# Kernel optimization log

Hardware: AMD Instinct MI355X
Metric: run time of the kernel (lower is better)

The kernel has to match this reference:

```python
import jax, jax.numpy as jnp
import numpy as np

B, S, H, I, A = 1024, 200, 256, 256, 128


def setup_inputs() -> dict:
    key = jax.random.key(0)
    ks = jax.random.split(key, 9)
    def xavier(k, shape):
        fan_in, fan_out = shape[1], shape[0]
        std = float(np.sqrt(2.0 / (fan_in + fan_out)))
        return jax.random.normal(k, shape, dtype=jnp.float32) * std
    return {
        "hidden_states": jax.random.normal(ks[0], (B, S, H), dtype=jnp.float32),
        "target_item": jax.random.normal(ks[1], (B, I), dtype=jnp.float32),
        "lengths": jax.random.randint(ks[2], (B,), 0, 201, dtype=jnp.int32),
        "W1": xavier(ks[3], (A, I + H)),
        "b1": jnp.zeros((A,), dtype=jnp.float32),
        "W2": xavier(ks[4], (1, A)),
        "Wr": xavier(ks[5], (H, I + H)),
        "br": jnp.zeros((H,), dtype=jnp.float32),
        "Wz": xavier(ks[6], (H, I + H)),
        "bz": jnp.zeros((H,), dtype=jnp.float32),
        "Wn": xavier(ks[7], (H, I + H)),
        "bn": jnp.zeros((H,), dtype=jnp.float32),
    }


def reference(hidden_states, target_item, lengths, W1, b1, W2, Wr, br, Wz, bz, Wn, bn):
    b, s, h = hidden_states.shape
    # attention scores over the sequence
    tgt = jnp.broadcast_to(target_item[:, None, :], (b, s, target_item.shape[-1]))
    combined = jnp.concatenate([hidden_states, tgt], axis=2)          # (B,S,2H)
    hid = jax.nn.relu(jnp.einsum('bsd,ad->bsa', combined, W1) + b1)   # (B,S,A)
    scores = jnp.einsum('bsa,oa->bs', hid, W2)                        # (B,S)
    mask = jnp.arange(s)[None, :] < lengths[:, None]
    scores = jnp.where(mask, scores, -1e9)
    att = jax.nn.softmax(scores, axis=1)                              # (B,S)

    def step(h_prev, xs):
        x, a = xs  # x: (B,I), a: (B,1)
        comb = jnp.concatenate([x, h_prev], axis=1)
        r = jax.nn.sigmoid(comb @ Wr.T + br)
        z = jax.nn.sigmoid(comb @ Wz.T + bz) * a
        comb_r = jnp.concatenate([x, r * h_prev], axis=1)
        n = jnp.tanh(comb_r @ Wn.T + bn)
        h_new = (1.0 - z) * h_prev + z * n
        return h_new, None

    h0 = jnp.zeros((b, h), dtype=hidden_states.dtype)
    xs = (jnp.transpose(hidden_states, (1, 0, 2)), att.T[:, :, None])  # (S,B,I),(S,B,1)
    h_final, _ = jax.lax.scan(step, h0, xs)
    return h_final
```

## Files before the change

kernel.cpp:

```cpp
#include <hip/hip_runtime.h>
#include <cstdint>

#define B_SZ  1024
#define S_LEN 200
#define H_DIM 256

typedef short s16x8 __attribute__((ext_vector_type(8)));
typedef float f32x4 __attribute__((ext_vector_type(4)));
typedef int   i32x4 __attribute__((ext_vector_type(4)));

__device__ __forceinline__ short f2bf(float f){
  uint32_t u = __float_as_uint(f);
  u += 0x7FFFu + ((u >> 16) & 1u);
  return (short)(u >> 16);
}
__device__ __forceinline__ float sigm(float x){
  return __fdividef(1.f, 1.f + __expf(-x));
}
__device__ __forceinline__ float tanh_f(float x){
  return 1.f - __fdividef(2.f, __expf(2.f*x) + 1.f);
}

__global__ __launch_bounds__(256) void prep_kernel(
    const float* __restrict__ Wr, const float* __restrict__ Wz,
    const float* __restrict__ Wn, const float* __restrict__ W1,
    short* __restrict__ wx, short* __restrict__ wrzh,
    short* __restrict__ wnh, short* __restrict__ w1b){
  const int NWX=196608, NRZ=131072, NN=65536;
  int i = blockIdx.x*256 + threadIdx.x;
  if(i < NWX){
    int o=i>>8, k=i&255;
    float v = (o<256)? Wr[o*512+k] : (o<512)? Wz[(o-256)*512+k] : Wn[(o-512)*512+k];
    wx[i]=f2bf(v);
  } else if(i < NWX+NRZ){
    int j=i-NWX; int o=j>>8, k=j&255;
    float v=(o<256)? Wr[o*512+256+k] : Wz[(o-256)*512+256+k];
    wrzh[j]=f2bf(v);
  } else if(i < NWX+NRZ+NN){
    int j=i-NWX-NRZ; int o=j>>8, k=j&255;
    wnh[j]=f2bf(Wn[o*512+256+k]);
  } else {
    int j=i-NWX-NRZ-NN;
    w1b[j]=f2bf(W1[j]);
  }
}

__global__ __launch_bounds__(256) void scores_kernel(
    const float* __restrict__ hs, const float* __restrict__ tgt,
    const short* __restrict__ w1, const float* __restrict__ b1,
    const float* __restrict__ w2, float* __restrict__ scores){
  const int tid = threadIdx.x;
  const int lane = tid & 63;
  const int wv  = tid >> 6;
  const int l15 = lane & 15;
  const int q   = lane >> 4;
  const int gw  = blockIdx.x * 4 + wv;
  float b1v[8], w2v[8];
  #pragma unroll
  for(int nt=0;nt<8;nt++){ b1v[nt]=b1[nt*16+l15]; w2v[nt]=w2[nt*16+l15]; }
  const short* w1p = w1 + (size_t)l15*512 + q*8;
  for(int it=0; it<2; it++){
    int mt0 = gw + it*3200;
    int mt1 = mt0 + 6400;
    int m0  = mt0*16 + l15;
    int m1  = mt1*16 + l15;
    int bA  = m0 / S_LEN, sA = m0 - bA*S_LEN;
    int bB  = m1 / S_LEN, sB = m1 - bB*S_LEN;
    const float* arowA = hs  + ((size_t)bA*S_LEN + sA)*H_DIM;
    const float* trowA = tgt + (size_t)bA*H_DIM;
    const float* arowB = hs  + ((size_t)bB*S_LEN + sB)*H_DIM;
    const float* trowB = tgt + (size_t)bB*H_DIM;
    f32x4 acc[2][8];
    #pragma unroll
    for(int u=0;u<2;u++)
      #pragma unroll
      for(int nt=0;nt<8;nt++) acc[u][nt] = (f32x4){0.f,0.f,0.f,0.f};
    for(int kt=0;kt<16;kt++){
      int k0 = kt*32 + q*8;
      const float* srcA = (k0 < H_DIM) ? (arowA + k0) : (trowA + (k0 - H_DIM));
      const float* srcB = (k0 < H_DIM) ? (arowB + k0) : (trowB + (k0 - H_DIM));
      float4 a0 = *(const float4*)(srcA);
      float4 a1 = *(const float4*)(srcA+4);
      float4 c0 = *(const float4*)(srcB);
      float4 c1 = *(const float4*)(srcB+4);
      s16x8 aA, aB;
      aA[0]=f2bf(a0.x); aA[1]=f2bf(a0.y); aA[2]=f2bf(a0.z); aA[3]=f2bf(a0.w);
      aA[4]=f2bf(a1.x); aA[5]=f2bf(a1.y); aA[6]=f2bf(a1.z); aA[7]=f2bf(a1.w);
      aB[0]=f2bf(c0.x); aB[1]=f2bf(c0.y); aB[2]=f2bf(c0.z); aB[3]=f2bf(c0.w);
      aB[4]=f2bf(c1.x); aB[5]=f2bf(c1.y); aB[6]=f2bf(c1.z); aB[7]=f2bf(c1.w);
      #pragma unroll
      for(int nt=0;nt<8;nt++){
        s16x8 bf = *(const s16x8*)(w1p + (size_t)nt*16*512 + kt*32);
        acc[0][nt] = __builtin_amdgcn_mfma_f32_16x16x32_bf16(aA, bf, acc[0][nt], 0, 0, 0);
        acc[1][nt] = __builtin_amdgcn_mfma_f32_16x16x32_bf16(aB, bf, acc[1][nt], 0, 0, 0);
      }
    }
    #pragma unroll
    for(int u=0;u<2;u++){
      float sr0=0.f, sr1=0.f, sr2=0.f, sr3=0.f;
      #pragma unroll
      for(int nt=0;nt<8;nt++){
        f32x4 h4 = acc[u][nt];
        sr0 += fmaxf(h4[0]+b1v[nt],0.f)*w2v[nt];
        sr1 += fmaxf(h4[1]+b1v[nt],0.f)*w2v[nt];
        sr2 += fmaxf(h4[2]+b1v[nt],0.f)*w2v[nt];
        sr3 += fmaxf(h4[3]+b1v[nt],0.f)*w2v[nt];
      }
      #pragma unroll
      for(int mask=1; mask<16; mask<<=1){
        sr0 += __shfl_xor(sr0, mask, 64);
        sr1 += __shfl_xor(sr1, mask, 64);
        sr2 += __shfl_xor(sr2, mask, 64);
        sr3 += __shfl_xor(sr3, mask, 64);
      }
      if(l15 < 4){
        float outv = (l15==0)?sr0:(l15==1)?sr1:(l15==2)?sr2:sr3;
        int mt = (u==0)?mt0:mt1;
        scores[(size_t)mt*16 + q*4 + l15] = outv;
      }
    }
  }
}

__global__ __launch_bounds__(256) void softmax_kernel(
    const float* __restrict__ scores, const int* __restrict__ lengths,
    float* __restrict__ att){
  const int b = blockIdx.x;
  const int s = threadIdx.x;
  const int lane = s & 63, wv = s >> 6;
  __shared__ float red[4];
  __shared__ float red2[4];
  float sc = -1e9f;
  if(s < S_LEN){
    float v = scores[(size_t)b*S_LEN + s];
    sc = (s < lengths[b]) ? v : -1e9f;
  }
  float mx = (s < S_LEN) ? sc : -INFINITY;
  #pragma unroll
  for(int mask=1; mask<64; mask<<=1) mx = fmaxf(mx, __shfl_xor(mx, mask, 64));
  if(lane==0) red[wv] = mx;
  __syncthreads();
  mx = fmaxf(fmaxf(red[0],red[1]), fmaxf(red[2],red[3]));
  float e = (s < S_LEN) ? expf(sc - mx) : 0.f;
  float sum = e;
  #pragma unroll
  for(int mask=1; mask<64; mask<<=1) sum += __shfl_xor(sum, mask, 64);
  if(lane==0) red2[wv] = sum;
  __syncthreads();
  sum = red2[0]+red2[1]+red2[2]+red2[3];
  if(s < S_LEN) att[(size_t)b*S_LEN + s] = e / sum;
}

__global__ __launch_bounds__(256) void xproj_kernel(
    const float* __restrict__ hs, const short* __restrict__ wx,
    const float* __restrict__ br, const float* __restrict__ bz,
    const float* __restrict__ bn, short* __restrict__ xpg){
  const int tid = threadIdx.x;
  const int lane = tid & 63;
  const int wv = tid >> 6;
  const int l15 = lane & 15;
  const int q = lane >> 4;
  const int wid = blockIdx.x*4 + wv;
  const int g = wid / 100;
  const int c = wid - g*100;
  s16x8 a[2][8];
  #pragma unroll
  for(int u=0;u<2;u++){
    const float* ap = hs + ((size_t)(g*16+l15)*S_LEN + (c*2+u))*H_DIM + q*8;
    #pragma unroll
    for(int kt=0;kt<8;kt++){
      f32x4 p0 = *(const f32x4*)(ap + kt*32);
      f32x4 p1 = *(const f32x4*)(ap + kt*32 + 4);
      s16x8 v;
      v[0]=f2bf(p0[0]); v[1]=f2bf(p0[1]); v[2]=f2bf(p0[2]); v[3]=f2bf(p0[3]);
      v[4]=f2bf(p1[0]); v[5]=f2bf(p1[1]); v[6]=f2bf(p1[2]); v[7]=f2bf(p1[3]);
      a[u][kt]=v;
    }
  }
  _Float16* xp = (_Float16*)xpg;
  const size_t Rbase = (size_t)g*3200 + (size_t)c*32;
  const short* wbase = wx + (size_t)l15*256 + q*8;
  for(int nt=0;nt<48;nt++){
    const short* wp = wbase + (size_t)nt*16*256;
    f32x4 acc0=(f32x4){0.f,0.f,0.f,0.f}, acc1=(f32x4){0.f,0.f,0.f,0.f};
    #pragma unroll
    for(int kt=0;kt<8;kt++){
      s16x8 bf = *(const s16x8*)(wp + kt*32);
      acc0 = __builtin_amdgcn_mfma_f32_16x16x32_bf16(a[0][kt],bf,acc0,0,0,0);
      acc1 = __builtin_amdgcn_mfma_f32_16x16x32_bf16(a[1][kt],bf,acc1,0,0,0);
    }
    int col = nt*16 + l15;
    const float* bp = (nt<16)? (br+nt*16) : (nt<32)? (bz+(nt-16)*16) : (bn+(nt-32)*16);
    float bv = bp[l15];
    #pragma unroll
    for(int reg=0;reg<4;reg++){
      xp[(Rbase      + q*4 + reg)*776 + col] = (_Float16)(acc0[reg] + bv);
      xp[(Rbase + 16 + q*4 + reg)*776 + col] = (_Float16)(acc1[reg] + bv);
    }
  }
}

__global__ __launch_bounds__(1024) void scan2_kernel(
    const short* __restrict__ xpg, const float* __restrict__ att,
    const short* __restrict__ wrzh, const short* __restrict__ wnh,
    float* __restrict__ out){
  __shared__ __align__(16) char smem[129024];
  short* comb0 = (short*)(smem + 99328);
  short* comb1 = (short*)(smem + 107776);
  float* attA  = (float*)(smem + 116224);

  const int tid = threadIdx.x;
  const int lane = tid & 63;
  const int wv  = tid >> 6;
  const int l15 = lane & 15;
  const int q   = lane >> 4;
  const int g   = blockIdx.x;
  const int b0  = g * 16;
  const int cX  = wv*16 + l15;

  s16x8 wfr[16], wfn[8];
  #pragma unroll
  for(int kt=0;kt<8;kt++){
    wfr[kt*2+0] = *(const s16x8*)(wrzh + (size_t)(cX      )*256 + kt*32 + q*8);
    wfr[kt*2+1] = *(const s16x8*)(wrzh + (size_t)(256 + cX)*256 + kt*32 + q*8);
    wfn[kt]     = *(const s16x8*)(wnh  + (size_t)(cX      )*256 + kt*32 + q*8);
  }
  float hreg[4];
  #pragma unroll
  for(int r2=0;r2<4;r2++) hreg[r2]=0.f;
  for(int i=tid;i<16*264;i+=1024) comb0[i]=0;
  for(int i=tid;i<16*S_LEN;i+=1024) attA[i]=att[(size_t)b0*S_LEN + i];
  {
    const char* gsrc = (const char*)xpg + (size_t)g*100*49664;
    i32x4 t0 = *(const i32x4*)(gsrc +         tid*16);
    i32x4 t1 = *(const i32x4*)(gsrc + 16384 + tid*16);
    i32x4 t2 = *(const i32x4*)(gsrc + 32768 + tid*16);
    *(i32x4*)(smem +         tid*16) = t0;
    *(i32x4*)(smem + 16384 + tid*16) = t1;
    *(i32x4*)(smem + 32768 + tid*16) = t2;
    if(tid<32){
      i32x4 t3 = *(const i32x4*)(gsrc + 49152 + tid*16);
      *(i32x4*)(smem + 49152 + tid*16) = t3;
    }
  }
  __syncthreads();

  int cur = 0;
  for(int c=0;c<100;c++){
    const _Float16* XPc = (const _Float16*)(smem + cur*49664);
    char* nb = smem + (cur^1)*49664;
    const char* gsrc = (const char*)xpg + (size_t)(g*100 + c + 1)*49664;
    const bool pf = (c+1 < 100);
    i32x4 v0, v1, v2, v3;
    if(pf){
      v0 = *(const i32x4*)(gsrc +         tid*16);
      v1 = *(const i32x4*)(gsrc + 16384 + tid*16);
    }
    #pragma unroll
    for(int tl=0;tl<2;tl++){
      const int t = c*2 + tl;
      f32x4 accR=(f32x4){0.f,0.f,0.f,0.f}, accZ=(f32x4){0.f,0.f,0.f,0.f};
      #pragma unroll
      for(int kt=0;kt<8;kt++){
        s16x8 a = *(const s16x8*)(comb0 + l15*264 + kt*32+q*8);
        accR=__builtin_amdgcn_mfma_f32_16x16x32_bf16(a,wfr[kt*2+0],accR,0,0,0);
        accZ=__builtin_amdgcn_mfma_f32_16x16x32_bf16(a,wfr[kt*2+1],accZ,0,0,0);
      }
      float zv[4];
      #pragma unroll
      for(int r2=0;r2<4;r2++){
        int row=q*4+r2;
        float xr = (float)XPc[(size_t)(tl*16+row)*776 +       cX];
        float xz = (float)XPc[(size_t)(tl*16+row)*776 + 256 + cX];
        float rg = sigm(accR[r2]+xr);
        comb1[row*264+cX] = f2bf(rg*hreg[r2]);
        zv[r2] = sigm(accZ[r2]+xz)*attA[row*S_LEN + t];
      }
      __syncthreads();
      if(pf){
        if(tl==0){
          *(i32x4*)(nb +         tid*16) = v0;
          *(i32x4*)(nb + 16384 + tid*16) = v1;
          v2 = *(const i32x4*)(gsrc + 32768 + tid*16);
          if(tid<32) v3 = *(const i32x4*)(gsrc + 49152 + tid*16);
        } else {
          *(i32x4*)(nb + 32768 + tid*16) = v2;
          if(tid<32) *(i32x4*)(nb + 49152 + tid*16) = v3;
        }
      }
      f32x4 acc2 = (f32x4){0.f,0.f,0.f,0.f};
      #pragma unroll
      for(int kt=0;kt<8;kt++){
        s16x8 a = *(const s16x8*)(comb1 + l15*264 + kt*32+q*8);
        acc2=__builtin_amdgcn_mfma_f32_16x16x32_bf16(a,wfn[kt],acc2,0,0,0);
      }
      #pragma unroll
      for(int r2=0;r2<4;r2++){
        int row=q*4+r2;
        float xn = (float)XPc[(size_t)(tl*16+row)*776 + 512 + cX];
        float nv = tanh_f(acc2[r2]+xn);
        hreg[r2] = fmaf(zv[r2], nv-hreg[r2], hreg[r2]);
        comb0[row*264+cX] = f2bf(hreg[r2]);
      }
      __syncthreads();
    }
    cur ^= 1;
  }
  #pragma unroll
  for(int r2=0;r2<4;r2++)
    out[(size_t)(b0 + q*4 + r2)*H_DIM + cX] = hreg[r2];
}

__global__ __launch_bounds__(1024) void scan_kernel(
    const float* __restrict__ hs, const float* __restrict__ att,
    const short* __restrict__ wx, const short* __restrict__ wrzh,
    const short* __restrict__ wnh,
    const float* __restrict__ br, const float* __restrict__ bz,
    const float* __restrict__ bn, float* __restrict__ out){
  __shared__ __align__(16) char smem[150272];
  _Float16* XP    = (_Float16*)smem;
  short*    xst   = (short*)(smem + 99328);
  short*    comb0 = (short*)(smem + 133120);
  short*    comb1 = (short*)(smem + 141568);
  float*    attc  = (float*)(smem + 150016);

  const int tid = threadIdx.x;
  const int lane = tid & 63;
  const int wv  = tid >> 6;
  const int l15 = lane & 15;
  const int q   = lane >> 4;
  const int b0  = blockIdx.x * 16;
  const int cX  = wv*16 + l15;

  s16x8 wfr[16], wfn[8];
  #pragma unroll
  for(int kt=0;kt<8;kt++){
    wfr[kt*2+0] = *(const s16x8*)(wrzh + (size_t)(cX      )*256 + kt*32 + q*8);
    wfr[kt*2+1] = *(const s16x8*)(wrzh + (size_t)(256 + cX)*256 + kt*32 + q*8);
    wfn[kt]     = *(const s16x8*)(wnh  + (size_t)(cX      )*256 + kt*32 + q*8);
  }
  float biasc[3];
  #pragma unroll
  for(int p=0;p<3;p++){
    int o=(wv*3+p)*16+l15;
    biasc[p] = (o<256)? br[o] : (o<512)? bz[o-256] : bn[o-512];
  }
  float hreg[4];
  #pragma unroll
  for(int r2=0;r2<4;r2++) hreg[r2]=0.f;
  for(int i=tid;i<16*264;i+=1024) comb0[i]=0;

  for(int c=0;c<50;c++){
    const int t0=c*4;
    #pragma unroll
    for(int jj=0;jj<2;jj++){
      int idx = tid + jj*1024;
      int r = idx>>5, k=(idx&31)*8;
      int bl=r&15, tl=r>>4;
      const float* src = hs + ((size_t)(b0+bl)*S_LEN + (t0+tl))*H_DIM + k;
      float4 v0=*(const float4*)src, v1=*(const float4*)(src+4);
      s16x8 xv;
      xv[0]=f2bf(v0.x); xv[1]=f2bf(v0.y); xv[2]=f2bf(v0.z); xv[3]=f2bf(v0.w);
      xv[4]=f2bf(v1.x); xv[5]=f2bf(v1.y); xv[6]=f2bf(v1.z); xv[7]=f2bf(v1.w);
      *(s16x8*)(xst + r*264 + k) = xv;
    }
    if(tid<64) attc[tid] = att[(size_t)(b0+(tid&15))*S_LEN + t0 + (tid>>4)];
    __syncthreads();
    #pragma unroll
    for(int p=0;p<3;p++){
      f32x4 xacc[4];
      #pragma unroll
      for(int tl=0;tl<4;tl++) xacc[tl]=(f32x4){0.f,0.f,0.f,0.f};
      #pragma unroll
      for(int kt=0;kt<8;kt++){
        s16x8 bf0 = *(const s16x8*)(wx + (size_t)((wv*3+p)*16+l15)*256 + kt*32+q*8);
        #pragma unroll
        for(int tl=0;tl<4;tl++){
          s16x8 a = *(const s16x8*)(xst + (tl*16+l15)*264 + kt*32 + q*8);
          xacc[tl]=__builtin_amdgcn_mfma_f32_16x16x32_bf16(a,bf0,xacc[tl],0,0,0);
        }
      }
      int col=(wv*3+p)*16+l15;
      float bias=biasc[p];
      #pragma unroll
      for(int tl=0;tl<4;tl++)
        #pragma unroll
        for(int reg=0;reg<4;reg++)
          XP[(size_t)(tl*16 + q*4+reg)*776 + col] = (_Float16)(xacc[tl][reg] + bias);
    }
    __syncthreads();
    for(int tl=0;tl<4;tl++){
      f32x4 accR=(f32x4){0.f,0.f,0.f,0.f}, accZ=(f32x4){0.f,0.f,0.f,0.f};
      #pragma unroll
      for(int kt=0;kt<8;kt++){
        s16x8 a = *(const s16x8*)(comb0 + l15*264 + kt*32+q*8);
        accR=__builtin_amdgcn_mfma_f32_16x16x32_bf16(a,wfr[kt*2+0],accR,0,0,0);
        accZ=__builtin_amdgcn_mfma_f32_16x16x32_bf16(a,wfr[kt*2+1],accZ,0,0,0);
      }
      float zv[4];
      #pragma unroll
      for(int r2=0;r2<4;r2++){
        int row=q*4+r2;
        float xr = (float)XP[(size_t)(tl*16+row)*776 +       cX];
        float xz = (float)XP[(size_t)(tl*16+row)*776 + 256 + cX];
        float rg = sigm(accR[r2]+xr);
        comb1[row*264+cX] = f2bf(rg*hreg[r2]);
        zv[r2] = sigm(accZ[r2]+xz)*attc[tl*16+row];
      }
      __syncthreads();
      f32x4 acc2 = (f32x4){0.f,0.f,0.f,0.f};
      #pragma unroll
      for(int kt=0;kt<8;kt++){
        s16x8 a = *(const s16x8*)(comb1 + l15*264 + kt*32+q*8);
        acc2=__builtin_amdgcn_mfma_f32_16x16x32_bf16(a,wfn[kt],acc2,0,0,0);
      }
      #pragma unroll
      for(int r2=0;r2<4;r2++){
        int row=q*4+r2;
        float xn = (float)XP[(size_t)(tl*16+row)*776 + 512 + cX];
        float nv = tanh_f(acc2[r2]+xn);
        hreg[r2] = fmaf(zv[r2], nv-hreg[r2], hreg[r2]);
        comb0[row*264+cX] = f2bf(hreg[r2]);
      }
      __syncthreads();
    }
  }
  #pragma unroll
  for(int r2=0;r2<4;r2++)
    out[(size_t)(b0 + q*4 + r2)*H_DIM + cX] = hreg[r2];
}

extern "C" void kernel_launch(void* const* d_in, const int* in_sizes, int n_in,
                              void* d_out, int out_size, void* d_ws, size_t ws_size,
                              hipStream_t stream) {
  const float* hs  = (const float*)d_in[0];
  const float* tgt = (const float*)d_in[1];
  const int*   len = (const int*)d_in[2];
  const float* W1  = (const float*)d_in[3];
  const float* b1  = (const float*)d_in[4];
  const float* W2  = (const float*)d_in[5];
  const float* Wr  = (const float*)d_in[6];
  const float* br  = (const float*)d_in[7];
  const float* Wz  = (const float*)d_in[8];
  const float* bz  = (const float*)d_in[9];
  const float* Wn  = (const float*)d_in[10];
  const float* bn  = (const float*)d_in[11];
  float* out = (float*)d_out;

  const size_t XPG_BYTES = (size_t)204800 * 776 * 2;
  const size_t NEED = XPG_BYTES + (size_t)458752*2 + (size_t)819200*2;
  if(ws_size >= NEED){
    short* xpgs = (short*)d_ws;
    short* wx   = (short*)((char*)d_ws + XPG_BYTES);
    short* wrzh = wx + 196608;
    short* wnh  = wrzh + 131072;
    short* w1b  = wnh + 65536;
    float* scores = (float*)(w1b + 65536);
    float* att    = scores + (size_t)B_SZ*S_LEN;
    prep_kernel<<<1792, 256, 0, stream>>>(Wr, Wz, Wn, W1, wx, wrzh, wnh, w1b);
    xproj_kernel<<<1600, 256, 0, stream>>>(hs, wx, br, bz, bn, xpgs);
    scores_kernel<<<800, 256, 0, stream>>>(hs, tgt, w1b, b1, W2, scores);
    softmax_kernel<<<1024, 256, 0, stream>>>(scores, len, att);
    scan2_kernel<<<64, 1024, 0, stream>>>(xpgs, att, wrzh, wnh, out);
  } else {
    short* wx   = (short*)d_ws;
    short* wrzh = wx + 196608;
    short* wnh  = wrzh + 131072;
    short* w1b  = wnh + 65536;
    float* scores = (float*)(w1b + 65536);
    float* att    = scores + (size_t)B_SZ*S_LEN;
    prep_kernel<<<1792, 256, 0, stream>>>(Wr, Wz, Wn, W1, wx, wrzh, wnh, w1b);
    scores_kernel<<<800, 256, 0, stream>>>(hs, tgt, w1b, b1, W2, scores);
    softmax_kernel<<<1024, 256, 0, stream>>>(scores, len, att);
    scan_kernel<<<64, 1024, 0, stream>>>(hs, att, wx, wrzh, wnh, br, bz, bn, out);
  }
}
```

Measured before the change: 1.679 ms.

## Interleave r/z/n input projections per column into padded 2-step chunks

The input-projection kernel now computes the r, z and n gates together per 16-column tile and stores them interleaved as four fp16 values per column, padded, in 64KB chunks covering two timesteps. The scan kernel double-buffers these chunks and reads all three gate inputs with one 8-byte LDS load, and xn is loaded early, before the second matmul. The point is to cut scattered 2-byte LDS reads and give aligned 16-byte chunk copies. In exchange the workspace grows (6400×64KB), chunk copies go up from 2 to 4 loads per thread, and the scan uses more shared memory. The fallback path now also needs the old projection workspace, since the fused scan_kernel was removed.

Result: slower. 1.906 ms (+13.5%).

```diff
diff --git a/kernel.cpp b/kernel.cpp
--- a/kernel.cpp
+++ b/kernel.cpp
@@ -6,6 +6,7 @@
 #define H_DIM 256
 
 typedef short s16x8 __attribute__((ext_vector_type(8)));
+typedef short s16x4 __attribute__((ext_vector_type(4)));
 typedef float f32x4 __attribute__((ext_vector_type(4)));
 typedef int   i32x4 __attribute__((ext_vector_type(4)));
 
@@ -13,6 +14,12 @@
   uint32_t u = __float_as_uint(f);
   u += 0x7FFFu + ((u >> 16) & 1u);
   return (short)(u >> 16);
+}
+__device__ __forceinline__ short f2h(float f){
+  union { _Float16 h; short s; } u; u.h = (_Float16)f; return u.s;
+}
+__device__ __forceinline__ float h2f(short s){
+  union { short s; _Float16 h; } u; u.s = s; return (float)u.h;
 }
 __device__ __forceinline__ float sigm(float x){
   return __fdividef(1.f, 1.f + __expf(-x));
@@ -151,7 +158,7 @@
   if(s < S_LEN) att[(size_t)b*S_LEN + s] = e / sum;
 }
 
-__global__ __launch_bounds__(256) void xproj_kernel(
+__global__ __launch_bounds__(256) void xproj2_kernel(
     const float* __restrict__ hs, const short* __restrict__ wx,
     const float* __restrict__ br, const float* __restrict__ bz,
     const float* __restrict__ bn, short* __restrict__ xpg){
@@ -177,6 +184,175 @@
       a[u][kt]=v;
     }
   }
+  char* chunk = (char*)xpg + (size_t)(g*100 + c)*65536;
+  const short* wbase = wx + (size_t)l15*256 + q*8;
+  for(int ct=0; ct<16; ct++){
+    int col = ct*16 + l15;
+    f32x4 ar0=(f32x4){0,0,0,0}, ar1=(f32x4){0,0,0,0};
+    f32x4 az0=(f32x4){0,0,0,0}, az1=(f32x4){0,0,0,0};
+    f32x4 an0=(f32x4){0,0,0,0}, an1=(f32x4){0,0,0,0};
+    const short* wr_ = wbase + (size_t)(      ct*16)*256;
+    const short* wz_ = wbase + (size_t)(256 + ct*16)*256;
+    const short* wn_ = wbase + (size_t)(512 + ct*16)*256;
+    #pragma unroll
+    for(int kt=0;kt<8;kt++){
+      s16x8 br_ = *(const s16x8*)(wr_ + kt*32);
+      s16x8 bz_ = *(const s16x8*)(wz_ + kt*32);
+      s16x8 bn_ = *(const s16x8*)(wn_ + kt*32);
+      ar0 = __builtin_amdgcn_mfma_f32_16x16x32_bf16(a[0][kt],br_,ar0,0,0,0);
+      ar1 = __builtin_amdgcn_mfma_f32_16x16x32_bf16(a[1][kt],br_,ar1,0,0,0);
+      az0 = __builtin_amdgcn_mfma_f32_16x16x32_bf16(a[0][kt],bz_,az0,0,0,0);
+      az1 = __builtin_amdgcn_mfma_f32_16x16x32_bf16(a[1][kt],bz_,az1,0,0,0);
+      an0 = __builtin_amdgcn_mfma_f32_16x16x32_bf16(a[0][kt],bn_,an0,0,0,0);
+      an1 = __builtin_amdgcn_mfma_f32_16x16x32_bf16(a[1][kt],bn_,an1,0,0,0);
+    }
+    float brv = br[col], bzv = bz[col], bnv = bn[col];
+    #pragma unroll
+    for(int reg=0;reg<4;reg++){
+      s16x4 p0, p1;
+      p0[0]=f2h(ar0[reg]+brv); p0[1]=f2h(az0[reg]+bzv); p0[2]=f2h(an0[reg]+bnv); p0[3]=0;
+      p1[0]=f2h(ar1[reg]+brv); p1[1]=f2h(az1[reg]+bzv); p1[2]=f2h(an1[reg]+bnv); p1[3]=0;
+      *(s16x4*)(chunk + (size_t)(     q*4+reg)*2048 + (size_t)col*8) = p0;
+      *(s16x4*)(chunk + (size_t)(16 + q*4+reg)*2048 + (size_t)col*8) = p1;
+    }
+  }
+}
+
+__global__ __launch_bounds__(1024) void scan2_kernel(
+    const short* __restrict__ xpg, const float* __restrict__ att,
+    const short* __restrict__ wrzh, const short* __restrict__ wnh,
+    float* __restrict__ out){
+  __shared__ __align__(16) char smem[160768];
+  short* comb0 = (short*)(smem + 131072);
+  short* comb1 = (short*)(smem + 139520);
+  float* attA  = (float*)(smem + 147968);
+
+  const int tid = threadIdx.x;
+  const int lane = tid & 63;
+  const int wv  = tid >> 6;
+  const int l15 = lane & 15;
+  const int q   = lane >> 4;
+  const int g   = blockIdx.x;
+  const int b0  = g * 16;
+  const int cX  = wv*16 + l15;
+
+  s16x8 wfr[16], wfn[8];
+  #pragma unroll
+  for(int kt=0;kt<8;kt++){
+    wfr[kt*2+0] = *(const s16x8*)(wrzh + (size_t)(cX      )*256 + kt*32 + q*8);
+    wfr[kt*2+1] = *(const s16x8*)(wrzh + (size_t)(256 + cX)*256 + kt*32 + q*8);
+    wfn[kt]     = *(const s16x8*)(wnh  + (size_t)(cX      )*256 + kt*32 + q*8);
+  }
+  float hreg[4];
+  #pragma unroll
+  for(int r2=0;r2<4;r2++) hreg[r2]=0.f;
+  for(int i=tid;i<16*264;i+=1024) comb0[i]=0;
+  for(int i=tid;i<16*S_LEN;i+=1024) attA[i]=att[(size_t)b0*S_LEN + i];
+  {
+    const char* gsrc = (const char*)xpg + (size_t)g*100*65536;
+    i32x4 t0 = *(const i32x4*)(gsrc +         tid*16);
+    i32x4 t1 = *(const i32x4*)(gsrc + 16384 + tid*16);
+    i32x4 t2 = *(const i32x4*)(gsrc + 32768 + tid*16);
+    i32x4 t3 = *(const i32x4*)(gsrc + 49152 + tid*16);
+    *(i32x4*)(smem +         tid*16) = t0;
+    *(i32x4*)(smem + 16384 + tid*16) = t1;
+    *(i32x4*)(smem + 32768 + tid*16) = t2;
+    *(i32x4*)(smem + 49152 + tid*16) = t3;
+  }
+  __syncthreads();
+
+  int cur = 0;
+  for(int c=0;c<100;c++){
+    const char* XPc = smem + cur*65536;
+    char* nb = smem + (cur^1)*65536;
+    const char* gsrc = (const char*)xpg + (size_t)(g*100 + c + 1)*65536;
+    const bool pf = (c+1 < 100);
+    i32x4 v0, v1, v2, v3;
+    if(pf){
+      v0 = *(const i32x4*)(gsrc +         tid*16);
+      v1 = *(const i32x4*)(gsrc + 16384 + tid*16);
+    }
+    #pragma unroll
+    for(int tl=0;tl<2;tl++){
+      const int t = c*2 + tl;
+      f32x4 accR=(f32x4){0.f,0.f,0.f,0.f}, accZ=(f32x4){0.f,0.f,0.f,0.f};
+      #pragma unroll
+      for(int kt=0;kt<8;kt++){
+        s16x8 a = *(const s16x8*)(comb0 + l15*264 + kt*32+q*8);
+        accR=__builtin_amdgcn_mfma_f32_16x16x32_bf16(a,wfr[kt*2+0],accR,0,0,0);
+        accZ=__builtin_amdgcn_mfma_f32_16x16x32_bf16(a,wfr[kt*2+1],accZ,0,0,0);
+      }
+      float zv[4], xnv[4];
+      #pragma unroll
+      for(int r2=0;r2<4;r2++){
+        int row=q*4+r2;
+        s16x4 xp4 = *(const s16x4*)(XPc + (size_t)(tl*16+row)*2048 + (size_t)cX*8);
+        float xr = h2f(xp4[0]);
+        float xz = h2f(xp4[1]);
+        xnv[r2]  = h2f(xp4[2]);
+        float rg = sigm(accR[r2]+xr);
+        comb1[row*264+cX] = f2bf(rg*hreg[r2]);
+        zv[r2] = sigm(accZ[r2]+xz)*attA[row*S_LEN + t];
+      }
+      __syncthreads();
+      if(pf){
+        if(tl==0){
+          *(i32x4*)(nb +         tid*16) = v0;
+          *(i32x4*)(nb + 16384 + tid*16) = v1;
+          v2 = *(const i32x4*)(gsrc + 32768 + tid*16);
+          v3 = *(const i32x4*)(gsrc + 49152 + tid*16);
+        } else {
+          *(i32x4*)(nb + 32768 + tid*16) = v2;
+          *(i32x4*)(nb + 49152 + tid*16) = v3;
+        }
+      }
+      f32x4 acc2 = (f32x4){0.f,0.f,0.f,0.f};
+      #pragma unroll
+      for(int kt=0;kt<8;kt++){
+        s16x8 a = *(const s16x8*)(comb1 + l15*264 + kt*32+q*8);
+        acc2=__builtin_amdgcn_mfma_f32_16x16x32_bf16(a,wfn[kt],acc2,0,0,0);
+      }
+      #pragma unroll
+      for(int r2=0;r2<4;r2++){
+        float nv = tanh_f(acc2[r2] + xnv[r2]);
+        hreg[r2] = fmaf(zv[r2], nv-hreg[r2], hreg[r2]);
+        comb0[(q*4+r2)*264+cX] = f2bf(hreg[r2]);
+      }
+      __syncthreads();
+    }
+    cur ^= 1;
+  }
+  #pragma unroll
+  for(int r2=0;r2<4;r2++)
+    out[(size_t)(b0 + q*4 + r2)*H_DIM + cX] = hreg[r2];
+}
+
+__global__ __launch_bounds__(256) void xproj_old_kernel(
+    const float* __restrict__ hs, const short* __restrict__ wx,
+    const float* __restrict__ br, const float* __restrict__ bz,
+    const float* __restrict__ bn, short* __restrict__ xpg){
+  const int tid = threadIdx.x;
+  const int lane = tid & 63;
+  const int wv = tid >> 6;
+  const int l15 = lane & 15;
+  const int q = lane >> 4;
+  const int wid = blockIdx.x*4 + wv;
+  const int g = wid / 100;
+  const int c = wid - g*100;
+  s16x8 a[2][8];
+  #pragma unroll
+  for(int u=0;u<2;u++){
+    const float* ap = hs + ((size_t)(g*16+l15)*S_LEN + (c*2+u))*H_DIM + q*8;
+    #pragma unroll
+    for(int kt=0;kt<8;kt++){
+      f32x4 p0 = *(const f32x4*)(ap + kt*32);
+      f32x4 p1 = *(const f32x4*)(ap + kt*32 + 4);
+      s16x8 v;
+      v[0]=f2bf(p0[0]); v[1]=f2bf(p0[1]); v[2]=f2bf(p0[2]); v[3]=f2bf(p0[3]);
+      v[4]=f2bf(p1[0]); v[5]=f2bf(p1[1]); v[6]=f2bf(p1[2]); v[7]=f2bf(p1[3]);
+      a[u][kt]=v;
+    }
+  }
   _Float16* xp = (_Float16*)xpg;
   const size_t Rbase = (size_t)g*3200 + (size_t)c*32;
   const short* wbase = wx + (size_t)l15*256 + q*8;
@@ -200,7 +376,7 @@
   }
 }
 
-__global__ __launch_bounds__(1024) void scan2_kernel(
+__global__ __launch_bounds__(1024) void scan2_old_kernel(
     const short* __restrict__ xpg, const float* __restrict__ att,
     const short* __restrict__ wrzh, const short* __restrict__ wnh,
     float* __restrict__ out){
@@ -298,126 +474,6 @@
       for(int r2=0;r2<4;r2++){
         int row=q*4+r2;
         float xn = (float)XPc[(size_t)(tl*16+row)*776 + 512 + cX];
-        float nv = tanh_f(acc2[r2]+xn);
-        hreg[r2] = fmaf(zv[r2], nv-hreg[r2], hreg[r2]);
-        comb0[row*264+cX] = f2bf(hreg[r2]);
-      }
-      __syncthreads();
-    }
-    cur ^= 1;
-  }
-  #pragma unroll
-  for(int r2=0;r2<4;r2++)
-    out[(size_t)(b0 + q*4 + r2)*H_DIM + cX] = hreg[r2];
-}
-
-__global__ __launch_bounds__(1024) void scan_kernel(
-    const float* __restrict__ hs, const float* __restrict__ att,
-    const short* __restrict__ wx, const short* __restrict__ wrzh,
-    const short* __restrict__ wnh,
-    const float* __restrict__ br, const float* __restrict__ bz,
-    const float* __restrict__ bn, float* __restrict__ out){
-  __shared__ __align__(16) char smem[150272];
-  _Float16* XP    = (_Float16*)smem;
-  short*    xst   = (short*)(smem + 99328);
-  short*    comb0 = (short*)(smem + 133120);
-  short*    comb1 = (short*)(smem + 141568);
-  float*    attc  = (float*)(smem + 150016);
-
-  const int tid = threadIdx.x;
-  const int lane = tid & 63;
-  const int wv  = tid >> 6;
-  const int l15 = lane & 15;
-  const int q   = lane >> 4;
-  const int b0  = blockIdx.x * 16;
-  const int cX  = wv*16 + l15;
-
-  s16x8 wfr[16], wfn[8];
-  #pragma unroll
-  for(int kt=0;kt<8;kt++){
-    wfr[kt*2+0] = *(const s16x8*)(wrzh + (size_t)(cX      )*256 + kt*32 + q*8);
-    wfr[kt*2+1] = *(const s16x8*)(wrzh + (size_t)(256 + cX)*256 + kt*32 + q*8);
-    wfn[kt]     = *(const s16x8*)(wnh  + (size_t)(cX      )*256 + kt*32 + q*8);
-  }
-  float biasc[3];
-  #pragma unroll
-  for(int p=0;p<3;p++){
-    int o=(wv*3+p)*16+l15;
-    biasc[p] = (o<256)? br[o] : (o<512)? bz[o-256] : bn[o-512];
-  }
-  float hreg[4];
-  #pragma unroll
-  for(int r2=0;r2<4;r2++) hreg[r2]=0.f;
-  for(int i=tid;i<16*264;i+=1024) comb0[i]=0;
-
-  for(int c=0;c<50;c++){
-    const int t0=c*4;
-    #pragma unroll
-    for(int jj=0;jj<2;jj++){
-      int idx = tid + jj*1024;
-      int r = idx>>5, k=(idx&31)*8;
-      int bl=r&15, tl=r>>4;
-      const float* src = hs + ((size_t)(b0+bl)*S_LEN + (t0+tl))*H_DIM + k;
-      float4 v0=*(const float4*)src, v1=*(const float4*)(src+4);
-      s16x8 xv;
-      xv[0]=f2bf(v0.x); xv[1]=f2bf(v0.y); xv[2]=f2bf(v0.z); xv[3]=f2bf(v0.w);
-      xv[4]=f2bf(v1.x); xv[5]=f2bf(v1.y); xv[6]=f2bf(v1.z); xv[7]=f2bf(v1.w);
-      *(s16x8*)(xst + r*264 + k) = xv;
-    }
-    if(tid<64) attc[tid] = att[(size_t)(b0+(tid&15))*S_LEN + t0 + (tid>>4)];
-    __syncthreads();
-    #pragma unroll
-    for(int p=0;p<3;p++){
-      f32x4 xacc[4];
-      #pragma unroll
-      for(int tl=0;tl<4;tl++) xacc[tl]=(f32x4){0.f,0.f,0.f,0.f};
-      #pragma unroll
-      for(int kt=0;kt<8;kt++){
-        s16x8 bf0 = *(const s16x8*)(wx + (size_t)((wv*3+p)*16+l15)*256 + kt*32+q*8);
-        #pragma unroll
-        for(int tl=0;tl<4;tl++){
-          s16x8 a = *(const s16x8*)(xst + (tl*16+l15)*264 + kt*32 + q*8);
-          xacc[tl]=__builtin_amdgcn_mfma_f32_16x16x32_bf16(a,bf0,xacc[tl],0,0,0);
-        }
-      }
-      int col=(wv*3+p)*16+l15;
-      float bias=biasc[p];
-      #pragma unroll
-      for(int tl=0;tl<4;tl++)
-        #pragma unroll
-        for(int reg=0;reg<4;reg++)
-          XP[(size_t)(tl*16 + q*4+reg)*776 + col] = (_Float16)(xacc[tl][reg] + bias);
-    }
-    __syncthreads();
-    for(int tl=0;tl<4;tl++){
-      f32x4 accR=(f32x4){0.f,0.f,0.f,0.f}, accZ=(f32x4){0.f,0.f,0.f,0.f};
-      #pragma unroll
-      for(int kt=0;kt<8;kt++){
-        s16x8 a = *(const s16x8*)(comb0 + l15*264 + kt*32+q*8);
-        accR=__builtin_amdgcn_mfma_f32_16x16x32_bf16(a,wfr[kt*2+0],accR,0,0,0);
-        accZ=__builtin_amdgcn_mfma_f32_16x16x32_bf16(a,wfr[kt*2+1],accZ,0,0,0);
-      }
-      float zv[4];
-      #pragma unroll
-      for(int r2=0;r2<4;r2++){
-        int row=q*4+r2;
-        float xr = (float)XP[(size_t)(tl*16+row)*776 +       cX];
-        float xz = (float)XP[(size_t)(tl*16+row)*776 + 256 + cX];
-        float rg = sigm(accR[r2]+xr);
-        comb1[row*264+cX] = f2bf(rg*hreg[r2]);
-        zv[r2] = sigm(accZ[r2]+xz)*attc[tl*16+row];
-      }
-      __syncthreads();
-      f32x4 acc2 = (f32x4){0.f,0.f,0.f,0.f};
-      #pragma unroll
-      for(int kt=0;kt<8;kt++){
-        s16x8 a = *(const s16x8*)(comb1 + l15*264 + kt*32+q*8);
-        acc2=__builtin_amdgcn_mfma_f32_16x16x32_bf16(a,wfn[kt],acc2,0,0,0);
-      }
-      #pragma unroll
-      for(int r2=0;r2<4;r2++){
-        int row=q*4+r2;
-        float xn = (float)XP[(size_t)(tl*16+row)*776 + 512 + cX];
         float nv = tanh_f(acc2[r2]+xn);
         hreg[r2] = fmaf(zv[r2], nv-hreg[r2], hreg[r2]);
         comb0[row*264+cX] = f2bf(hreg[r2]);
@@ -447,31 +503,34 @@
   const float* bn  = (const float*)d_in[11];
   float* out = (float*)d_out;
 
-  const size_t XPG_BYTES = (size_t)204800 * 776 * 2;
-  const size_t NEED = XPG_BYTES + (size_t)458752*2 + (size_t)819200*2;
-  if(ws_size >= NEED){
+  const size_t WTS = (size_t)458752*2 + (size_t)819200*2;
+  const size_t XPG2_BYTES = (size_t)6400 * 65536;
+  const size_t XPG1_BYTES = (size_t)204800 * 776 * 2;
+  if(ws_size >= XPG2_BYTES + WTS){
     short* xpgs = (short*)d_ws;
-    short* wx   = (short*)((char*)d_ws + XPG_BYTES);
+    short* wx   = (short*)((char*)d_ws + XPG2_BYTES);
     short* wrzh = wx + 196608;
     short* wnh  = wrzh + 131072;
     short* w1b  = wnh + 65536;
     float* scores = (float*)(w1b + 65536);
     float* att    = scores + (size_t)B_SZ*S_LEN;
     prep_kernel<<<1792, 256, 0, stream>>>(Wr, Wz, Wn, W1, wx, wrzh, wnh, w1b);
-    xproj_kernel<<<1600, 256, 0, stream>>>(hs, wx, br, bz, bn, xpgs);
+    xproj2_kernel<<<1600, 256, 0, stream>>>(hs, wx, br, bz, bn, xpgs);
     scores_kernel<<<800, 256, 0, stream>>>(hs, tgt, w1b, b1, W2, scores);
     softmax_kernel<<<1024, 256, 0, stream>>>(scores, len, att);
     scan2_kernel<<<64, 1024, 0, stream>>>(xpgs, att, wrzh, wnh, out);
   } else {
-    short* wx   = (short*)d_ws;
+    short* xpgs = (short*)d_ws;
+    short* wx   = (short*)((char*)d_ws + XPG1_BYTES);
     short* wrzh = wx + 196608;
     short* wnh  = wrzh + 131072;
     short* w1b  = wnh + 65536;
     float* scores = (float*)(w1b + 65536);
     float* att    = scores + (size_t)B_SZ*S_LEN;
     prep_kernel<<<1792, 256, 0, stream>>>(Wr, Wz, Wn, W1, wx, wrzh, wnh, w1b);
+    xproj_old_kernel<<<1600, 256, 0, stream>>>(hs, wx, br, bz, bn, xpgs);
     scores_kernel<<<800, 256, 0, stream>>>(hs, tgt, w1b, b1, W2, scores);
     softmax_kernel<<<1024, 256, 0, stream>>>(scores, len, att);
-    scan_kernel<<<64, 1024, 0, stream>>>(hs, att, wx, wrzh, wnh, br, bz, bn, out);
-  }
-}
+    scan2_old_kernel<<<64, 1024, 0, stream>>>(xpgs, att, wrzh, wnh, out);
+  }
+}
```

## Stage input-projection weights in swizzled LDS shared by 16 waves per block

Applied to the files above, without the earlier changes.

The input-projection kernel now runs 1024-thread blocks that cooperatively load the bf16 weight matrix into double-buffered, XOR-swizzled shared memory in 32-row slices. All 16 waves reuse each slice instead of every wave streaming the full weights from global/L2. The next slice is prefetched into registers while the current one is used. The fallback scan_kernel path for small workspaces is removed, so the large workspace is now assumed to be available.

New measurement: 1.613 ms. 1.04x faster.

```diff
diff --git a/kernel.cpp b/kernel.cpp
--- a/kernel.cpp
+++ b/kernel.cpp
@@ -151,16 +151,17 @@
   if(s < S_LEN) att[(size_t)b*S_LEN + s] = e / sum;
 }
 
-__global__ __launch_bounds__(256) void xproj_kernel(
+__global__ __launch_bounds__(1024) void xproj3_kernel(
     const float* __restrict__ hs, const short* __restrict__ wx,
     const float* __restrict__ br, const float* __restrict__ bz,
     const float* __restrict__ bn, short* __restrict__ xpg){
+  __shared__ __align__(16) short stg[2][6*16*256];
   const int tid = threadIdx.x;
   const int lane = tid & 63;
   const int wv = tid >> 6;
   const int l15 = lane & 15;
   const int q = lane >> 4;
-  const int wid = blockIdx.x*4 + wv;
+  const int wid = blockIdx.x*16 + wv;
   const int g = wid / 100;
   const int c = wid - g*100;
   s16x8 a[2][8];
@@ -177,25 +178,76 @@
       a[u][kt]=v;
     }
   }
+  i32x4 st[3];
+  #pragma unroll
+  for(int j=0;j<3;j++){
+    int w = tid + j*1024;
+    int m = w>>10, rem = w&1023, rr = rem>>5, kc = rem&31;
+    st[j] = *(const i32x4*)(wx + ((size_t)(m<<8) + rr)*256 + kc*8);
+  }
+  #pragma unroll
+  for(int j=0;j<3;j++){
+    int w = tid + j*1024;
+    int m = w>>10, rem = w&1023, rr = rem>>5, kc = rem&31;
+    *(i32x4*)(&stg[0][((m*2+(rr>>4))*16 + (rr&15))*256 + (kc^(rr&7))*8]) = st[j];
+  }
+  __syncthreads();
+
+  const size_t Rbase = (size_t)g*3200 + (size_t)c*32;
   _Float16* xp = (_Float16*)xpg;
-  const size_t Rbase = (size_t)g*3200 + (size_t)c*32;
-  const short* wbase = wx + (size_t)l15*256 + q*8;
-  for(int nt=0;nt<48;nt++){
-    const short* wp = wbase + (size_t)nt*16*256;
-    f32x4 acc0=(f32x4){0.f,0.f,0.f,0.f}, acc1=(f32x4){0.f,0.f,0.f,0.f};
-    #pragma unroll
-    for(int kt=0;kt<8;kt++){
-      s16x8 bf = *(const s16x8*)(wp + kt*32);
-      acc0 = __builtin_amdgcn_mfma_f32_16x16x32_bf16(a[0][kt],bf,acc0,0,0,0);
-      acc1 = __builtin_amdgcn_mfma_f32_16x16x32_bf16(a[1][kt],bf,acc1,0,0,0);
-    }
-    int col = nt*16 + l15;
-    const float* bp = (nt<16)? (br+nt*16) : (nt<32)? (bz+(nt-16)*16) : (bn+(nt-32)*16);
-    float bv = bp[l15];
-    #pragma unroll
-    for(int reg=0;reg<4;reg++){
-      xp[(Rbase      + q*4 + reg)*776 + col] = (_Float16)(acc0[reg] + bv);
-      xp[(Rbase + 16 + q*4 + reg)*776 + col] = (_Float16)(acc1[reg] + bv);
+  for(int s=0;s<8;s++){
+    const short* sb = stg[s&1];
+    if(s<7){
+      #pragma unroll
+      for(int j=0;j<3;j++){
+        int w = tid + j*1024;
+        int m = w>>10, rem = w&1023, rr = rem>>5, kc = rem&31;
+        st[j] = *(const i32x4*)(wx + ((size_t)(m<<8) + (s+1)*32 + rr)*256 + kc*8);
+      }
+    }
+    #pragma unroll
+    for(int cc=0;cc<2;cc++){
+      int ct = s*2+cc;
+      f32x4 ar0=(f32x4){0,0,0,0}, ar1=(f32x4){0,0,0,0};
+      f32x4 az0=(f32x4){0,0,0,0}, az1=(f32x4){0,0,0,0};
+      f32x4 an0=(f32x4){0,0,0,0}, an1=(f32x4){0,0,0,0};
+      #pragma unroll
+      for(int kt=0;kt<8;kt++){
+        int ch = ((kt*4+q) ^ (l15&7))*8;
+        s16x8 br_ = *(const s16x8*)(sb + ((0+cc)*16 + l15)*256 + ch);
+        s16x8 bz_ = *(const s16x8*)(sb + ((2+cc)*16 + l15)*256 + ch);
+        s16x8 bn_ = *(const s16x8*)(sb + ((4+cc)*16 + l15)*256 + ch);
+        ar0 = __builtin_amdgcn_mfma_f32_16x16x32_bf16(a[0][kt],br_,ar0,0,0,0);
+        ar1 = __builtin_amdgcn_mfma_f32_16x16x32_bf16(a[1][kt],br_,ar1,0,0,0);
+        az0 = __builtin_amdgcn_mfma_f32_16x16x32_bf16(a[0][kt],bz_,az0,0,0,0);
+        az1 = __builtin_amdgcn_mfma_f32_16x16x32_bf16(a[1][kt],bz_,az1,0,0,0);
+        an0 = __builtin_amdgcn_mfma_f32_16x16x32_bf16(a[0][kt],bn_,an0,0,0,0);
+        an1 = __builtin_amdgcn_mfma_f32_16x16x32_bf16(a[1][kt],bn_,an1,0,0,0);
+      }
+      int col = ct*16 + l15;
+      float brv = br[col], bzv = bz[col], bnv = bn[col];
+      #pragma unroll
+      for(int reg=0;reg<4;reg++){
+        size_t r0 = (Rbase      + q*4 + reg)*776;
+        size_t r1 = (Rbase + 16 + q*4 + reg)*776;
+        xp[r0 +       col] = (_Float16)(ar0[reg] + brv);
+        xp[r0 + 256 + col] = (_Float16)(az0[reg] + bzv);
+        xp[r0 + 512 + col] = (_Float16)(an0[reg] + bnv);
+        xp[r1 +       col] = (_Float16)(ar1[reg] + brv);
+        xp[r1 + 256 + col] = (_Float16)(az1[reg] + bzv);
+        xp[r1 + 512 + col] = (_Float16)(an1[reg] + bnv);
+      }
+    }
+    __syncthreads();
+    if(s<7){
+      short* nbuf = stg[(s+1)&1];
+      #pragma unroll
+      for(int j=0;j<3;j++){
+        int w = tid + j*1024;
+        int m = w>>10, rem = w&1023, rr = rem>>5, kc = rem&31;
+        *(i32x4*)(&nbuf[((m*2+(rr>>4))*16 + (rr&15))*256 + (kc^(rr&7))*8]) = st[j];
+      }
+      __syncthreads();
     }
   }
 }
@@ -305,125 +357,6 @@
       __syncthreads();
     }
     cur ^= 1;
-  }
-  #pragma unroll
-  for(int r2=0;r2<4;r2++)
-    out[(size_t)(b0 + q*4 + r2)*H_DIM + cX] = hreg[r2];
-}
-
-__global__ __launch_bounds__(1024) void scan_kernel(
-    const float* __restrict__ hs, const float* __restrict__ att,
-    const short* __restrict__ wx, const short* __restrict__ wrzh,
-    const short* __restrict__ wnh,
-    const float* __restrict__ br, const float* __restrict__ bz,
-    const float* __restrict__ bn, float* __restrict__ out){
-  __shared__ __align__(16) char smem[150272];
-  _Float16* XP    = (_Float16*)smem;
-  short*    xst   = (short*)(smem + 99328);
-  short*    comb0 = (short*)(smem + 133120);
-  short*    comb1 = (short*)(smem + 141568);
-  float*    attc  = (float*)(smem + 150016);
-
-  const int tid = threadIdx.x;
-  const int lane = tid & 63;
-  const int wv  = tid >> 6;
-  const int l15 = lane & 15;
-  const int q   = lane >> 4;
-  const int b0  = blockIdx.x * 16;
-  const int cX  = wv*16 + l15;
-
-  s16x8 wfr[16], wfn[8];
-  #pragma unroll
-  for(int kt=0;kt<8;kt++){
-    wfr[kt*2+0] = *(const s16x8*)(wrzh + (size_t)(cX      )*256 + kt*32 + q*8);
-    wfr[kt*2+1] = *(const s16x8*)(wrzh + (size_t)(256 + cX)*256 + kt*32 + q*8);
-    wfn[kt]     = *(const s16x8*)(wnh  + (size_t)(cX      )*256 + kt*32 + q*8);
-  }
-  float biasc[3];
-  #pragma unroll
-  for(int p=0;p<3;p++){
-    int o=(wv*3+p)*16+l15;
-    biasc[p] = (o<256)? br[o] : (o<512)? bz[o-256] : bn[o-512];
-  }
-  float hreg[4];
-  #pragma unroll
-  for(int r2=0;r2<4;r2++) hreg[r2]=0.f;
-  for(int i=tid;i<16*264;i+=1024) comb0[i]=0;
-
-  for(int c=0;c<50;c++){
-    const int t0=c*4;
-    #pragma unroll
-    for(int jj=0;jj<2;jj++){
-      int idx = tid + jj*1024;
-      int r = idx>>5, k=(idx&31)*8;
-      int bl=r&15, tl=r>>4;
-      const float* src = hs + ((size_t)(b0+bl)*S_LEN + (t0+tl))*H_DIM + k;
-      float4 v0=*(const float4*)src, v1=*(const float4*)(src+4);
-      s16x8 xv;
-      xv[0]=f2bf(v0.x); xv[1]=f2bf(v0.y); xv[2]=f2bf(v0.z); xv[3]=f2bf(v0.w);
-      xv[4]=f2bf(v1.x); xv[5]=f2bf(v1.y); xv[6]=f2bf(v1.z); xv[7]=f2bf(v1.w);
-      *(s16x8*)(xst + r*264 + k) = xv;
-    }
-    if(tid<64) attc[tid] = att[(size_t)(b0+(tid&15))*S_LEN + t0 + (tid>>4)];
-    __syncthreads();
-    #pragma unroll
-    for(int p=0;p<3;p++){
-      f32x4 xacc[4];
-      #pragma unroll
-      for(int tl=0;tl<4;tl++) xacc[tl]=(f32x4){0.f,0.f,0.f,0.f};
-      #pragma unroll
-      for(int kt=0;kt<8;kt++){
-        s16x8 bf0 = *(const s16x8*)(wx + (size_t)((wv*3+p)*16+l15)*256 + kt*32+q*8);
-        #pragma unroll
-        for(int tl=0;tl<4;tl++){
-          s16x8 a = *(const s16x8*)(xst + (tl*16+l15)*264 + kt*32 + q*8);
-          xacc[tl]=__builtin_amdgcn_mfma_f32_16x16x32_bf16(a,bf0,xacc[tl],0,0,0);
-        }
-      }
-      int col=(wv*3+p)*16+l15;
-      float bias=biasc[p];
-      #pragma unroll
-      for(int tl=0;tl<4;tl++)
-        #pragma unroll
-        for(int reg=0;reg<4;reg++)
-          XP[(size_t)(tl*16 + q*4+reg)*776 + col] = (_Float16)(xacc[tl][reg] + bias);
-    }
-    __syncthreads();
-    for(int tl=0;tl<4;tl++){
-      f32x4 accR=(f32x4){0.f,0.f,0.f,0.f}, accZ=(f32x4){0.f,0.f,0.f,0.f};
-      #pragma unroll
-      for(int kt=0;kt<8;kt++){
-        s16x8 a = *(const s16x8*)(comb0 + l15*264 + kt*32+q*8);
-        accR=__builtin_amdgcn_mfma_f32_16x16x32_bf16(a,wfr[kt*2+0],accR,0,0,0);
-        accZ=__builtin_amdgcn_mfma_f32_16x16x32_bf16(a,wfr[kt*2+1],accZ,0,0,0);
-      }
-      float zv[4];
-      #pragma unroll
-      for(int r2=0;r2<4;r2++){
-        int row=q*4+r2;
-        float xr = (float)XP[(size_t)(tl*16+row)*776 +       cX];
-        float xz = (float)XP[(size_t)(tl*16+row)*776 + 256 + cX];
-        float rg = sigm(accR[r2]+xr);
-        comb1[row*264+cX] = f2bf(rg*hreg[r2]);
-        zv[r2] = sigm(accZ[r2]+xz)*attc[tl*16+row];
-      }
-      __syncthreads();
-      f32x4 acc2 = (f32x4){0.f,0.f,0.f,0.f};
-      #pragma unroll
-      for(int kt=0;kt<8;kt++){
-        s16x8 a = *(const s16x8*)(comb1 + l15*264 + kt*32+q*8);
-        acc2=__builtin_amdgcn_mfma_f32_16x16x32_bf16(a,wfn[kt],acc2,0,0,0);
-      }
-      #pragma unroll
-      for(int r2=0;r2<4;r2++){
-        int row=q*4+r2;
-        float xn = (float)XP[(size_t)(tl*16+row)*776 + 512 + cX];
-        float nv = tanh_f(acc2[r2]+xn);
-        hreg[r2] = fmaf(zv[r2], nv-hreg[r2], hreg[r2]);
-        comb0[row*264+cX] = f2bf(hreg[r2]);
-      }
-      __syncthreads();
-    }
   }
   #pragma unroll
   for(int r2=0;r2<4;r2++)
@@ -447,31 +380,17 @@
   const float* bn  = (const float*)d_in[11];
   float* out = (float*)d_out;
 
-  const size_t XPG_BYTES = (size_t)204800 * 776 * 2;
-  const size_t NEED = XPG_BYTES + (size_t)458752*2 + (size_t)819200*2;
-  if(ws_size >= NEED){
-    short* xpgs = (short*)d_ws;
-    short* wx   = (short*)((char*)d_ws + XPG_BYTES);
-    short* wrzh = wx + 196608;
-    short* wnh  = wrzh + 131072;
-    short* w1b  = wnh + 65536;
-    float* scores = (float*)(w1b + 65536);
-    float* att    = scores + (size_t)B_SZ*S_LEN;
-    prep_kernel<<<1792, 256, 0, stream>>>(Wr, Wz, Wn, W1, wx, wrzh, wnh, w1b);
-    xproj_kernel<<<1600, 256, 0, stream>>>(hs, wx, br, bz, bn, xpgs);
-    scores_kernel<<<800, 256, 0, stream>>>(hs, tgt, w1b, b1, W2, scores);
-    softmax_kernel<<<1024, 256, 0, stream>>>(scores, len, att);
-    scan2_kernel<<<64, 1024, 0, stream>>>(xpgs, att, wrzh, wnh, out);
-  } else {
-    short* wx   = (short*)d_ws;
-    short* wrzh = wx + 196608;
-    short* wnh  = wrzh + 131072;
-    short* w1b  = wnh + 65536;
-    float* scores = (float*)(w1b + 65536);
-    float* att    = scores + (size_t)B_SZ*S_LEN;
-    prep_kernel<<<1792, 256, 0, stream>>>(Wr, Wz, Wn, W1, wx, wrzh, wnh, w1b);
-    scores_kernel<<<800, 256, 0, stream>>>(hs, tgt, w1b, b1, W2, scores);
-    softmax_kernel<<<1024, 256, 0, stream>>>(scores, len, att);
-    scan_kernel<<<64, 1024, 0, stream>>>(hs, att, wx, wrzh, wnh, br, bz, bn, out);
-  }
-}
+  const size_t XPG1_BYTES = (size_t)204800 * 776 * 2;
+  short* xpgs = (short*)d_ws;
+  short* wx   = (short*)((char*)d_ws + XPG1_BYTES);
+  short* wrzh = wx + 196608;
+  short* wnh  = wrzh + 131072;
+  short* w1b  = wnh + 65536;
+  float* scores = (float*)(w1b + 65536);
+  float* att    = scores + (size_t)B_SZ*S_LEN;
+  prep_kernel<<<1792, 256, 0, stream>>>(Wr, Wz, Wn, W1, wx, wrzh, wnh, w1b);
+  xproj3_kernel<<<400, 1024, 0, stream>>>(hs, wx, br, bz, bn, xpgs);
+  scores_kernel<<<800, 256, 0, stream>>>(hs, tgt, w1b, b1, W2, scores);
+  softmax_kernel<<<1024, 256, 0, stream>>>(scores, len, att);
+  scan2_kernel<<<64, 1024, 0, stream>>>(xpgs, att, wrzh, wnh, out);
+}
```
